# Kernel tuning notes

Hardware: AMD Instinct MI355X
Metric: run time of the kernel (lower is better)

Reference implementation:

```python
import jax, jax.numpy as jnp
import numpy as np

B, S, D, H, SKG = 4, 1024, 1024, 16, 256
HD = D // H  # head dim = 64


def setup_inputs() -> dict:
    key = jax.random.key(0)
    ks = jax.random.split(key, 8)
    std = 0.02
    return {
        "x": jax.random.normal(ks[0], (B, S, D), dtype=jnp.float32),
        "pred_kg": jax.random.normal(ks[1], (B, SKG, D), dtype=jnp.float32),
        "Wc": jax.random.normal(ks[2], (D, 3 * D), dtype=jnp.float32) * std,  # c_attn weight
        "bc": jnp.zeros((3 * D,), dtype=jnp.float32),
        "Wk": jax.random.normal(ks[3], (D, 2 * D), dtype=jnp.float32) * std,  # k_attn weight
        "bk": jnp.zeros((2 * D,), dtype=jnp.float32),
        "Wp": jax.random.normal(ks[4], (D, D), dtype=jnp.float32) * std,     # c_proj weight (shared)
        "bp": jnp.zeros((D,), dtype=jnp.float32),
    }


def _split_heads(t):  # [B, T, D] -> [B, H, T, HD]
    Bb, T, _ = t.shape
    return t.reshape(Bb, T, H, HD).transpose(0, 2, 1, 3)


def _merge_heads(t):  # [B, H, T, HD] -> [B, T, D]
    Bb, _, T, _ = t.shape
    return t.transpose(0, 2, 1, 3).reshape(Bb, T, D)


def reference(x, pred_kg, Wc, bc, Wk, bk, Wp, bp):
    # ---- self-attention branch (GPT-2 style, explicit causal bias blend) ----
    qkv = x @ Wc + bc                       # Conv1D: [B,S,3D]
    q, k, v = jnp.split(qkv, 3, axis=-1)
    q = _split_heads(q)                     # [B,H,S,HD]
    k = _split_heads(k)
    v = _split_heads(v)

    inv_sqrt_d = 1.0 / jnp.sqrt(jnp.float32(HD))
    w = jnp.einsum("bhqd,bhkd->bhqk", q, k) * inv_sqrt_d  # [B,H,S,S]
    causal = jnp.tril(jnp.ones((S, S), dtype=w.dtype))    # bias buffer slice b
    # faithful to: w = w * b - 10000.0 * (1 - b)
    w = w * causal - 10000.0 * (1.0 - causal)
    w = jax.nn.softmax(w, axis=-1)
    a = jnp.einsum("bhqk,bhkd->bhqd", w, v)
    a = _merge_heads(a) @ Wp + bp           # c_proj; resid dropout is identity in eval

    # ---- KG cross-attention branch (shares query and c_proj) ----
    kkv = pred_kg @ Wk + bk                 # [B,SKG,2D]
    kk, kv = jnp.split(kkv, 2, axis=-1)
    kk = _split_heads(kk)                   # [B,H,SKG,HD]
    kv = _split_heads(kv)
    w2 = jnp.einsum("bhqd,bhkd->bhqk", q, kk) * inv_sqrt_d  # [B,H,S,SKG]
    w2 = jax.nn.softmax(w2, axis=-1)
    ka = jnp.einsum("bhqk,bhkd->bhqd", w2, kv)
    ka = _merge_heads(ka) @ Wp + bp

    # concat the two branch outputs along the sequence axis: [B, S+SKG, D]
    return jnp.concatenate([a, ka], axis=1)
```

## Files before the change

kernel.cpp:

```cpp
#include <hip/hip_runtime.h>
#include <hip/hip_bf16.h>

typedef __bf16 bf16_t;
typedef bf16_t bf16x8 __attribute__((ext_vector_type(8)));
typedef bf16_t bf16x4 __attribute__((ext_vector_type(4)));
typedef float f32x4 __attribute__((ext_vector_type(4)));
typedef float f32x16 __attribute__((ext_vector_type(16)));

#define EXP2C 0.1803368867f
#define FEXP2(x) __builtin_amdgcn_exp2f(x)

__device__ __forceinline__ void gload16(const void* g, void* l) {
  __builtin_amdgcn_global_load_lds(
      (const __attribute__((address_space(1))) void*)g,
      (__attribute__((address_space(3))) void*)l, 16, 0, 0);
}

__device__ __forceinline__ unsigned pkbf(float lo, float hi) {
  unsigned short a = __builtin_bit_cast(unsigned short, (bf16_t)lo);
  unsigned short b = __builtin_bit_cast(unsigned short, (bf16_t)hi);
  return (unsigned)a | ((unsigned)b << 16);
}

__device__ __forceinline__ void plswap(unsigned& a, unsigned& b) {
#if __has_builtin(__builtin_amdgcn_permlane32_swap)
  auto r = __builtin_amdgcn_permlane32_swap(a, b, false, false);
  a = r[0]; b = r[1];
#else
  asm("v_permlane32_swap_b32 %0, %1" : "+v"(a), "+v"(b));
#endif
}
__device__ __forceinline__ float xmax32(float x) {
  unsigned a = __builtin_bit_cast(unsigned, x), b = a;
  plswap(a, b);
  return fmaxf(__builtin_bit_cast(float, a), __builtin_bit_cast(float, b));
}
__device__ __forceinline__ float xsum32(float x) {
  unsigned a = __builtin_bit_cast(unsigned, x), b = a;
  plswap(a, b);
  return __builtin_bit_cast(float, a) + __builtin_bit_cast(float, b);
}

__global__ __launch_bounds__(256) void prep_kernel(
    const float* __restrict__ x, bf16_t* __restrict__ xb,
    const float* __restrict__ pkg, bf16_t* __restrict__ pkb,
    const float* __restrict__ Wc, bf16_t* __restrict__ Wct,
    const float* __restrict__ Wk, bf16_t* __restrict__ Wkt,
    const float* __restrict__ Wp, bf16_t* __restrict__ Wpt) {
  __shared__ float tile[32][33];
  const int bid = blockIdx.x, tid = threadIdx.x;
  if (bid < 5120) {
    int i = bid * 256 + tid;
    const float* src; bf16_t* dst;
    if (i < 1048576) { src = x; dst = xb; }
    else { i -= 1048576; src = pkg; dst = pkb; }
    float4 v = reinterpret_cast<const float4*>(src)[i];
    bf16x4 o = { (bf16_t)v.x, (bf16_t)v.y, (bf16_t)v.z, (bf16_t)v.w };
    reinterpret_cast<bf16x4*>(dst)[i] = o;
    return;
  }
  int r = bid - 5120;
  int xx = r % 192, ky = r / 192;
  const float* W; bf16_t* T; int N;
  if (xx < 96) { W = Wc; T = Wct; N = 3072; }
  else if (xx < 160) { W = Wk; T = Wkt; N = 2048; xx -= 96; }
  else { W = Wp; T = Wpt; N = 1024; xx -= 160; }
  const int K = 1024;
  int tx = tid & 31, ty = tid >> 5;
  int n0 = xx * 32, k0 = ky * 32;
#pragma unroll
  for (int i = 0; i < 4; ++i)
    tile[ty + i * 8][tx] = W[(size_t)(k0 + ty + i * 8) * N + n0 + tx];
  __syncthreads();
#pragma unroll
  for (int i = 0; i < 4; ++i)
    T[(size_t)(n0 + ty + i * 8) * K + k0 + tx] = (bf16_t)tile[tx][ty + i * 8];
}

__global__ __launch_bounds__(256) void pack2_kernel(
    const bf16_t* __restrict__ src0, bf16_t* __restrict__ kd0, bf16_t* __restrict__ vd0,
    const bf16_t* __restrict__ src1, bf16_t* __restrict__ kd1, bf16_t* __restrict__ vd1) {
  __shared__ bf16_t vt[32][72];
  const int tid = threadIdx.x;
  int x = blockIdx.x;
  const int bh = blockIdx.y;
  const bf16_t* src; bf16_t *kd, *vd; int R, stride, kcol, vcol, NT, t;
  if (x < 32) { src = src0; kd = kd0; vd = vd0; R = 1024; stride = 3072; kcol = 1024; vcol = 2048; NT = 32; t = x; }
  else        { src = src1; kd = kd1; vd = vd1; R = 256;  stride = 2048; kcol = 0;    vcol = 1024; NT = 8;  t = x - 32; }
  const int b = bh >> 4, h = bh & 15;
  const size_t srow = (size_t)b * R + t * 32;
  const size_t obase = ((size_t)bh * NT + t) * 2048;
  {
    int r = tid >> 3, c = tid & 7;
    bf16x8 d = *(const bf16x8*)&src[(srow + r) * stride + vcol + h * 64 + c * 8];
    *(bf16x8*)&vt[r][c * 8] = d;
  }
  {
    int ks = tid >> 6, l = tid & 63;
    int hi8 = (l >> 5) * 8;
    bf16x8 d = *(const bf16x8*)&src[(srow + (l & 31)) * stride + kcol + h * 64 + ks * 16 + hi8];
    *(bf16x8*)&kd[obase + ks * 512 + l * 8] = d;
  }
  __syncthreads();
  {
    int dd = tid >> 6, l = tid & 63;
    int mb = dd >> 1, ks = dd & 1;
    int hd = mb * 32 + (l & 31);
    int kvr = ks * 16 + (l >> 5) * 8;
    bf16x8 o;
#pragma unroll
    for (int j = 0; j < 8; ++j) o[j] = vt[kvr + j][hd];
    *(bf16x8*)&vd[obase + dd * 512 + l * 8] = o;
  }
}

#define MFMA2(mi, ni)                                                         \
  acc[mi][ni] = __builtin_amdgcn_mfma_f32_16x16x32_bf16(af[(mi) & 1][0], bf[ni][0], acc[mi][ni], 0, 0, 0); \
  acc[mi][ni] = __builtin_amdgcn_mfma_f32_16x16x32_bf16(af[(mi) & 1][1], bf[ni][1], acc[mi][ni], 0, 0, 0);
#define MFMA8(qm, qn)                                                         \
  MFMA2(2 * (qm) + 0, 2 * (qn) + 0) MFMA2(2 * (qm) + 0, 2 * (qn) + 1)         \
  MFMA2(2 * (qm) + 1, 2 * (qn) + 0) MFMA2(2 * (qm) + 1, 2 * (qn) + 1)
#define GBAR() __builtin_amdgcn_s_barrier()
#define LGKM0() asm volatile("s_waitcnt lgkmcnt(0)" ::: "memory")

template <int OUTF32>
__device__ __forceinline__ void gemm8_body(
    char* smem, const bf16_t* __restrict__ A, const bf16_t* __restrict__ Bt,
    const float* __restrict__ bias, void* __restrict__ Cout,
    int N, int K, int bx, int by) {
  const int tid = threadIdx.x;
  const int l = tid & 63, w = tid >> 6;
  const int lr = l & 15, lg = l >> 4;
  const int m0 = by * 256, n0 = bx * 128;
  const int wr = (w >> 1) * 64, wc = (w & 1) * 64;

  const int sr = tid >> 3;
  const int scb = ((tid & 7) * 16) ^ ((sr & 7) << 4);
  const bf16_t* Ab = A + (size_t)m0 * K + (scb >> 1);
  const bf16_t* Bb = Bt + (size_t)n0 * K + (scb >> 1);
  const int nk = K >> 6;

  const int hA = w >> 2;
  const int rA = ((w >> 1) & 1) * 64 + lr;
  const int rB = wc + lr;
  const int xr = (lr & 7) << 4;

  auto STAGE_A = [&](int t, int h) {
    const bf16_t* g = Ab + (size_t)(h * 128 + sr) * K + t * 64;
    char* d = smem + ((size_t)(t & 1) * 2 + h) * 16384 + tid * 16;
    gload16(g, d);
    gload16(g + (size_t)64 * K, d + 8192);
  };
  auto STAGE_B = [&](int t) {
    const bf16_t* g = Bb + (size_t)sr * K + t * 64;
    char* d = smem + 65536 + (size_t)(t & 1) * 16384 + tid * 16;
    gload16(g, d);
    gload16(g + (size_t)64 * K, d + 8192);
  };

  f32x4 acc[4][4] = {};
  bf16x8 af[2][2], bf[4][2];

  STAGE_A(0, 0); STAGE_A(0, 1); STAGE_B(0); STAGE_B(1); STAGE_A(1, 0);
  asm volatile("s_waitcnt vmcnt(4)" ::: "memory");
  GBAR();

  for (int t = 0; t < nk; ++t) {
    const char* pA = smem + ((size_t)(t & 1) * 2 + hA) * 16384;
    const char* pB = smem + 65536 + (size_t)(t & 1) * 16384;
    auto LDA = [&](int mf, int ks) {
      return *(const bf16x8*)(pA + (rA + mf * 16) * 128 + ((ks * 64 + lg * 16) ^ xr));
    };
    auto LDB = [&](int nf, int ks) {
      return *(const bf16x8*)(pB + (rB + nf * 16) * 128 + ((ks * 64 + lg * 16) ^ xr));
    };
    af[0][0] = LDA(0, 0); af[0][1] = LDA(0, 1);
    af[1][0] = LDA(1, 0); af[1][1] = LDA(1, 1);
    bf[0][0] = LDB(0, 0); bf[0][1] = LDB(0, 1);
    bf[1][0] = LDB(1, 0); bf[1][1] = LDB(1, 1);
    if (t + 1 < nk) STAGE_A(t + 1, 1);
    GBAR(); LGKM0();
    __builtin_amdgcn_s_setprio(1);
    MFMA8(0, 0)
    __builtin_amdgcn_s_setprio(0);
    GBAR();
    bf[2][0] = LDB(2, 0); bf[2][1] = LDB(2, 1);
    bf[3][0] = LDB(3, 0); bf[3][1] = LDB(3, 1);
    GBAR(); LGKM0();
    __builtin_amdgcn_s_setprio(1);
    MFMA8(0, 1)
    __builtin_amdgcn_s_setprio(0);
    GBAR();
    af[0][0] = LDA(2, 0); af[0][1] = LDA(2, 1);
    af[1][0] = LDA(3, 0); af[1][1] = LDA(3, 1);
    if (t + 2 < nk) STAGE_B(t + 2);
    GBAR(); LGKM0();
    __builtin_amdgcn_s_setprio(1);
    MFMA8(1, 0)
    __builtin_amdgcn_s_setprio(0);
    GBAR();
    if (t + 2 < nk) STAGE_A(t + 2, 0);
    GBAR();
    __builtin_amdgcn_s_setprio(1);
    MFMA8(1, 1)
    __builtin_amdgcn_s_setprio(0);
    if (t + 2 < nk)      asm volatile("s_waitcnt vmcnt(4)" ::: "memory");
    else if (t + 1 < nk) asm volatile("s_waitcnt vmcnt(0)" ::: "memory");
    GBAR();
  }

#pragma unroll
  for (int mf = 0; mf < 4; ++mf) {
#pragma unroll
    for (int nf = 0; nf < 4; ++nf) {
      int col = n0 + wc + nf * 16 + lr;
      float bb = bias[col];
      int rowb = m0 + wr + mf * 16 + lg * 4;
#pragma unroll
      for (int r = 0; r < 4; ++r) {
        float v = acc[mf][nf][r] + bb;
        if constexpr (OUTF32)
          ((float*)Cout)[(size_t)(rowb + r) * N + col] = v;
        else
          ((bf16_t*)Cout)[(size_t)(rowb + r) * N + col] = (bf16_t)v;
      }
    }
  }
}

__global__ __launch_bounds__(512, 1) void gemm2_kernel(
    const bf16_t* __restrict__ A0, const bf16_t* __restrict__ B0,
    const float* __restrict__ bi0, bf16_t* __restrict__ C0,
    const bf16_t* __restrict__ A1, const bf16_t* __restrict__ B1,
    const float* __restrict__ bi1, bf16_t* __restrict__ C1) {
  extern __shared__ char smem[];
  int bid = blockIdx.x;
  int wg = (bid & 7) * 56 + (bid >> 3);
  if (wg < 384)
    gemm8_body<0>(smem, A0, B0, bi0, C0, 3072, 1024, wg % 24, wg / 24);
  else {
    int r = wg - 384;
    gemm8_body<0>(smem, A1, B1, bi1, C1, 2048, 1024, r % 16, r / 16);
  }
}

__global__ __launch_bounds__(512, 1) void gemm_proj_kernel(
    const bf16_t* __restrict__ A, const bf16_t* __restrict__ Bt,
    const float* __restrict__ bias, float* __restrict__ Cout) {
  extern __shared__ char smem[];
  int bid = blockIdx.x;
  int wg = (bid & 7) * 32 + (bid >> 3);
  gemm8_body<1>(smem, A, Bt, bias, Cout, 1024, 1024, wg % 8, wg / 8);
}

#define STAGE(bf, t)                                                         \
  {                                                                          \
    gload16(kba + (size_t)(t) * 2048 + tid * 8, &sKV[bf][tid * 16]);         \
    gload16(vba + (size_t)(t) * 2048 + tid * 8, &sKV[bf][4096 + tid * 16]);  \
  }
#define QKT()                                                                \
  {                                                                          \
    __builtin_amdgcn_s_setprio(1);                                           \
    _Pragma("unroll") for (int ks = 0; ks < 4; ++ks)                         \
        sa = __builtin_amdgcn_mfma_f32_32x32x16_bf16(kf[ks], qf[ks], sa, 0, 0, 0); \
    __builtin_amdgcn_s_setprio(0);                                           \
  }
#define SMPV(vf, tcur)                                                       \
  {                                                                          \
    float sv[16];                                                            \
    const bool mt = is_self && ((tcur) == qw);                               \
    _Pragma("unroll") for (int r = 0; r < 16; ++r) {                         \
      float v = sa[r];                                                       \
      if (mt) {                                                              \
        int kvr = (r & 3) + 8 * (r >> 2) + kv4;                              \
        v = (kvr > ql) ? -1e30f : v;                                         \
      }                                                                      \
      sv[r] = v;                                                             \
    }                                                                        \
    float tm = fmaxf(                                                        \
        fmaxf(fmaxf(fmaxf(sv[0], sv[1]), fmaxf(sv[2], sv[3])),               \
              fmaxf(fmaxf(sv[4], sv[5]), fmaxf(sv[6], sv[7]))),              \
        fmaxf(fmaxf(fmaxf(sv[8], sv[9]), fmaxf(sv[10], sv[11])),             \
              fmaxf(fmaxf(sv[12], sv[13]), fmaxf(sv[14], sv[15]))));         \
    tm = xmax32(tm);                                                         \
    if (!__all(tm <= mcur + 64.f)) {                                         \
      float mn = fmaxf(mcur, tm);                                            \
      float sc = FEXP2((mcur - mn) * EXP2C);                                 \
      mcur = mn;                                                             \
      lcur *= sc;                                                            \
      _Pragma("unroll") for (int mb = 0; mb < 2; ++mb)                       \
          _Pragma("unroll") for (int r = 0; r < 16; ++r) oacc[mb][r] *= sc;  \
    }                                                                        \
    const float hm = mcur * EXP2C;                                           \
    float pf[16];                                                            \
    _Pragma("unroll") for (int r = 0; r < 16; ++r)                           \
        pf[r] = FEXP2(__builtin_fmaf(sv[r], EXP2C, -hm));                    \
    float ps = (((pf[0] + pf[1]) + (pf[2] + pf[3])) +                        \
                ((pf[4] + pf[5]) + (pf[6] + pf[7]))) +                       \
               (((pf[8] + pf[9]) + (pf[10] + pf[11])) +                      \
                ((pf[12] + pf[13]) + (pf[14] + pf[15])));                    \
    ps = xsum32(ps);                                                         \
    lcur += ps;                                                              \
    unsigned o01 = pkbf(pf[0], pf[1]), o23 = pkbf(pf[2], pf[3]);             \
    unsigned o45 = pkbf(pf[4], pf[5]), o67 = pkbf(pf[6], pf[7]);             \
    unsigned o89 = pkbf(pf[8], pf[9]), o1011 = pkbf(pf[10], pf[11]);         \
    unsigned o1213 = pkbf(pf[12], pf[13]), o1415 = pkbf(pf[14], pf[15]);     \
    plswap(o01, o45); plswap(o23, o67);                                      \
    plswap(o89, o1213); plswap(o1011, o1415);                                \
    uint4 w0 = { o01, o23, o45, o67 };                                       \
    uint4 w1 = { o89, o1011, o1213, o1415 };                                 \
    bf16x8 pb0 = __builtin_bit_cast(bf16x8, w0);                             \
    bf16x8 pb1 = __builtin_bit_cast(bf16x8, w1);                             \
    __builtin_amdgcn_s_setprio(1);                                           \
    oacc[0] = __builtin_amdgcn_mfma_f32_32x32x16_bf16(vf[0], pb0, oacc[0], 0, 0, 0); \
    oacc[0] = __builtin_amdgcn_mfma_f32_32x32x16_bf16(vf[1], pb1, oacc[0], 0, 0, 0); \
    oacc[1] = __builtin_amdgcn_mfma_f32_32x32x16_bf16(vf[2], pb0, oacc[1], 0, 0, 0); \
    oacc[1] = __builtin_amdgcn_mfma_f32_32x32x16_bf16(vf[3], pb1, oacc[1], 0, 0, 0); \
    __builtin_amdgcn_s_setprio(0);                                           \
  }

__global__ __launch_bounds__(256) void attn_kernel(
    const bf16_t* __restrict__ qkv,
    const bf16_t* __restrict__ kfs, const bf16_t* __restrict__ vfs,
    const bf16_t* __restrict__ kfc, const bf16_t* __restrict__ vfc,
    bf16_t* __restrict__ obuf) {
  __shared__ __align__(16) char sKV[3][8192];

  const int tid = threadIdx.x;
  const int w = tid >> 6, l = tid & 63;
  const int ql = l & 31;
  const bool uhi = l >= 32;
  const int kv4 = uhi ? 4 : 0;
  const int hi8 = uhi ? 8 : 0;

  const int bid = blockIdx.x;
  const bool is_self = bid < 512;
  int qb, bh, nt;
  if (is_self) {
    qb = 7 - (bid >> 6);
    bh = bid & 63;
    nt = qb * 4 + 4;
  } else {
    int cb = bid - 512;
    qb = cb >> 6;
    bh = cb & 63;
    nt = 8;
  }
  const int qw = qb * 4 + w;
  const int b = bh >> 4, h = bh & 15;
  const int hcol = h * 64;
  const int q0 = qw * 32;
  const int tlim = is_self ? qw : (nt - 1);

  const bf16_t* kba; const bf16_t* vba; int ooff;
  if (is_self) {
    kba = kfs + (size_t)bh * 32 * 2048; vba = vfs + (size_t)bh * 32 * 2048; ooff = 0;
  } else {
    kba = kfc + (size_t)bh * 8 * 2048;  vba = vfc + (size_t)bh * 8 * 2048;  ooff = 1024;
  }

  const bf16_t* qrow = qkv + (size_t)(b * 1024 + q0 + ql) * 3072 + hcol + hi8;
  bf16x8 qf[4];
#pragma unroll
  for (int ks = 0; ks < 4; ++ks) qf[ks] = *(const bf16x8*)(qrow + ks * 16);

  float mcur = -1e30f, lcur = 0.f;
  f32x16 oacc[2] = {};

  STAGE(0, 0); STAGE(1, 1);
  asm volatile("s_waitcnt vmcnt(2)" ::: "memory");
  __builtin_amdgcn_s_barrier();

  int cur = 0;
  for (int t = 0; t < nt; ++t) {
    int s2 = cur + 2; if (s2 >= 3) s2 -= 3;
    if (t + 2 < nt) STAGE(s2, t + 2);
    if (t <= tlim) {
      bf16x8 kf[4], vf[4];
#pragma unroll
      for (int c = 0; c < 4; ++c)
        kf[c] = *(const bf16x8*)&sKV[cur][c * 1024 + l * 16];
#pragma unroll
      for (int c = 0; c < 4; ++c)
        vf[c] = *(const bf16x8*)&sKV[cur][4096 + c * 1024 + l * 16];
      f32x16 sa = {};
      QKT();
      SMPV(vf, t);
    }
    if (t + 2 < nt)      asm volatile("s_waitcnt vmcnt(2)" ::: "memory");
    else if (t + 1 < nt) asm volatile("s_waitcnt vmcnt(0)" ::: "memory");
    __builtin_amdgcn_s_barrier();
    cur = cur + 1; if (cur >= 3) cur -= 3;
  }
  __syncthreads();

  const float rl = 1.0f / lcur;
  char* swp = &sKV[0][0] + w * 4096;
#pragma unroll
  for (int mb = 0; mb < 2; ++mb)
#pragma unroll
    for (int r2 = 0; r2 < 8; ++r2) {
      float lo = oacc[mb][2 * r2] * rl;
      float hiv = oacc[mb][2 * r2 + 1] * rl;
      int hdb = (r2 & 1) * 2 + 8 * (r2 >> 1) + kv4 + mb * 32;
      int off = (ql * 128 + hdb * 2) ^ ((ql & 7) << 4);
      *(unsigned*)(swp + off) = pkbf(lo, hiv);
    }
  __syncthreads();
  const int orow = b * 2048 + ooff + q0;
#pragma unroll
  for (int it = 0; it < 4; ++it) {
    int idx = it * 64 + l;
    int q = idx >> 3, ch = idx & 7;
    int off = (q * 128 + ch * 16) ^ ((q & 7) << 4);
    uint4 d = *(uint4*)(swp + off);
    *(uint4*)&obuf[(size_t)(orow + q) * 1024 + hcol + ch * 8] = d;
  }
}

extern "C" void kernel_launch(void* const* d_in, const int* in_sizes, int n_in,
                              void* d_out, int out_size, void* d_ws, size_t ws_size,
                              hipStream_t stream) {
  (void)in_sizes; (void)n_in; (void)out_size; (void)ws_size;
  const float* x   = (const float*)d_in[0];
  const float* pkg = (const float*)d_in[1];
  const float* Wc  = (const float*)d_in[2];
  const float* bc  = (const float*)d_in[3];
  const float* Wk  = (const float*)d_in[4];
  const float* bk  = (const float*)d_in[5];
  const float* Wp  = (const float*)d_in[6];
  const float* bp  = (const float*)d_in[7];
  float* out = (float*)d_out;

  char* ws = (char*)d_ws;
  const size_t MB = 1u << 20;
  bf16_t* xb   = (bf16_t*)(ws + 0 * MB);
  bf16_t* pkb  = (bf16_t*)(ws + 8 * MB);
  bf16_t* Wct  = (bf16_t*)(ws + 10 * MB);
  bf16_t* Wkt  = (bf16_t*)(ws + 16 * MB);
  bf16_t* Wpt  = (bf16_t*)(ws + 20 * MB);
  bf16_t* kkvb = (bf16_t*)(ws + 22 * MB);
  bf16_t* abuf = (bf16_t*)(ws + 26 * MB);
  bf16_t* vfs  = (bf16_t*)(ws + 0 * MB);
  bf16_t* kfc  = (bf16_t*)(ws + 8 * MB);
  bf16_t* vfc  = (bf16_t*)(ws + 10 * MB);
  bf16_t* qkvb = (bf16_t*)d_out;
  bf16_t* kfs  = (bf16_t*)((char*)d_out + 24 * MB);

  prep_kernel<<<11264, 256, 0, stream>>>(x, xb, pkg, pkb, Wc, Wct, Wk, Wkt, Wp, Wpt);
  gemm2_kernel<<<448, 512, 98304, stream>>>(xb, Wct, bc, qkvb, pkb, Wkt, bk, kkvb);
  pack2_kernel<<<dim3(40, 64), 256, 0, stream>>>(qkvb, kfs, vfs, kkvb, kfc, vfc);
  attn_kernel<<<1024, 256, 0, stream>>>(qkvb, kfs, vfs, kfc, vfc, abuf);
  gemm_proj_kernel<<<256, 512, 98304, stream>>>(abuf, Wpt, bp, out);
}
```

Measured before the change: 114.7 us.

## Use 256x256 tiles for the QKV and KG projection GEMM

Replaces the 256x128-tile GEMM used for the fused QKV/KKV projection with a new 256x256-tile body. Each wave computes a 128x64 sub-tile in four quadrant phases, staging A and B halves into double-buffered LDS with prioritized MFMA sections. The grid halves from 448 to 224 workgroups and LDS grows to 128KB. The larger tile raises arithmetic intensity and cuts redundant global loads, but 224 blocks is fewer than the 256 CUs on MI355X, so some CUs sit idle.

After: 110.6 us. -3.6%, faster.

```diff
diff --git a/kernel.cpp b/kernel.cpp
--- a/kernel.cpp
+++ b/kernel.cpp
@@ -114,14 +114,150 @@
   }
 }
 
+#define GBAR() __builtin_amdgcn_s_barrier()
+#define LGKM0() asm volatile("s_waitcnt lgkmcnt(0)" ::: "memory")
+
+__device__ __forceinline__ void gemm256_body(
+    char* smem, const bf16_t* __restrict__ A, const bf16_t* __restrict__ Bt,
+    const float* __restrict__ bias, bf16_t* __restrict__ Cout,
+    int N, int K, int bx, int by) {
+  const int tid = threadIdx.x;
+  const int l = tid & 63, w = tid >> 6;
+  const int lr = l & 15, lg = l >> 4;
+  const int m0 = by * 256, n0 = bx * 256;
+  const int wr = (w >> 2) * 128, wc = (w & 3) * 64;
+  const int hA = w >> 2, hB = (w >> 1) & 1;
+
+  const int sr = tid >> 3;
+  const int scb = ((tid & 7) * 16) ^ ((sr & 7) << 4);
+  const bf16_t* Ab = A + (size_t)m0 * K + (scb >> 1);
+  const bf16_t* Bb = Bt + (size_t)n0 * K + (scb >> 1);
+  const int nk = K >> 6;
+  const int xr = (lr & 7) << 4;
+
+  auto STAGE_A = [&](int t, int h) {
+    const bf16_t* g = Ab + (size_t)(h * 128 + sr) * K + t * 64;
+    char* d = smem + ((size_t)(t & 1) * 2 + h) * 16384 + tid * 16;
+    gload16(g, d);
+    gload16(g + (size_t)64 * K, d + 8192);
+  };
+  auto STAGE_B = [&](int t, int h) {
+    const bf16_t* g = Bb + (size_t)(h * 128 + sr) * K + t * 64;
+    char* d = smem + 65536 + ((size_t)(t & 1) * 2 + h) * 16384 + tid * 16;
+    gload16(g, d);
+    gload16(g + (size_t)64 * K, d + 8192);
+  };
+
+  f32x4 acc[8][4] = {};
+  bf16x8 af[4][2], bf[2][2][2];
+
+  STAGE_A(0, 0); STAGE_A(0, 1); STAGE_B(0, 0); STAGE_B(0, 1);
+  asm volatile("s_waitcnt vmcnt(0)" ::: "memory");
+  GBAR();
+
+  for (int t = 0; t < nk; ++t) {
+    const char* pA = smem + ((size_t)(t & 1) * 2 + hA) * 16384;
+    const char* pB = smem + 65536 + ((size_t)(t & 1) * 2 + hB) * 16384;
+    auto LDA = [&](int mf, int ks) {
+      return *(const bf16x8*)(pA + (mf * 16 + lr) * 128 + ((ks * 64 + lg * 16) ^ xr));
+    };
+    auto LDB = [&](int nf, int ks) {
+      return *(const bf16x8*)(pB + ((w & 1) * 64 + nf * 16 + lr) * 128 + ((ks * 64 + lg * 16) ^ xr));
+    };
+#pragma unroll
+    for (int mf = 0; mf < 4; ++mf) { af[mf][0] = LDA(mf, 0); af[mf][1] = LDA(mf, 1); }
+#pragma unroll
+    for (int nf = 0; nf < 2; ++nf) { bf[0][nf][0] = LDB(nf, 0); bf[0][nf][1] = LDB(nf, 1); }
+    if (t + 1 < nk) { STAGE_A(t + 1, 0); STAGE_B(t + 1, 0); }
+    GBAR(); LGKM0();
+    __builtin_amdgcn_s_setprio(1);
+#pragma unroll
+    for (int mf = 0; mf < 4; ++mf)
+#pragma unroll
+      for (int nf = 0; nf < 2; ++nf) {
+        acc[mf][nf] = __builtin_amdgcn_mfma_f32_16x16x32_bf16(af[mf][0], bf[0][nf][0], acc[mf][nf], 0, 0, 0);
+        acc[mf][nf] = __builtin_amdgcn_mfma_f32_16x16x32_bf16(af[mf][1], bf[0][nf][1], acc[mf][nf], 0, 0, 0);
+      }
+    __builtin_amdgcn_s_setprio(0);
+    GBAR();
+#pragma unroll
+    for (int nf = 0; nf < 2; ++nf) { bf[1][nf][0] = LDB(2 + nf, 0); bf[1][nf][1] = LDB(2 + nf, 1); }
+    if (t + 1 < nk) { STAGE_A(t + 1, 1); STAGE_B(t + 1, 1); }
+    GBAR(); LGKM0();
+    __builtin_amdgcn_s_setprio(1);
+#pragma unroll
+    for (int mf = 0; mf < 4; ++mf)
+#pragma unroll
+      for (int nf = 0; nf < 2; ++nf) {
+        acc[mf][2 + nf] = __builtin_amdgcn_mfma_f32_16x16x32_bf16(af[mf][0], bf[1][nf][0], acc[mf][2 + nf], 0, 0, 0);
+        acc[mf][2 + nf] = __builtin_amdgcn_mfma_f32_16x16x32_bf16(af[mf][1], bf[1][nf][1], acc[mf][2 + nf], 0, 0, 0);
+      }
+    __builtin_amdgcn_s_setprio(0);
+    GBAR();
+#pragma unroll
+    for (int mf = 0; mf < 4; ++mf) { af[mf][0] = LDA(4 + mf, 0); af[mf][1] = LDA(4 + mf, 1); }
+    GBAR(); LGKM0();
+    __builtin_amdgcn_s_setprio(1);
+#pragma unroll
+    for (int mf = 0; mf < 4; ++mf)
+#pragma unroll
+      for (int nf = 0; nf < 2; ++nf) {
+        acc[4 + mf][nf] = __builtin_amdgcn_mfma_f32_16x16x32_bf16(af[mf][0], bf[0][nf][0], acc[4 + mf][nf], 0, 0, 0);
+        acc[4 + mf][nf] = __builtin_amdgcn_mfma_f32_16x16x32_bf16(af[mf][1], bf[0][nf][1], acc[4 + mf][nf], 0, 0, 0);
+      }
+    __builtin_amdgcn_s_setprio(0);
+    GBAR();
+    __builtin_amdgcn_s_setprio(1);
+#pragma unroll
+    for (int mf = 0; mf < 4; ++mf)
+#pragma unroll
+      for (int nf = 0; nf < 2; ++nf) {
+        acc[4 + mf][2 + nf] = __builtin_amdgcn_mfma_f32_16x16x32_bf16(af[mf][0], bf[1][nf][0], acc[4 + mf][2 + nf], 0, 0, 0);
+        acc[4 + mf][2 + nf] = __builtin_amdgcn_mfma_f32_16x16x32_bf16(af[mf][1], bf[1][nf][1], acc[4 + mf][2 + nf], 0, 0, 0);
+      }
+    __builtin_amdgcn_s_setprio(0);
+    asm volatile("s_waitcnt vmcnt(0)" ::: "memory");
+    GBAR();
+  }
+
+#pragma unroll
+  for (int mf = 0; mf < 8; ++mf) {
+#pragma unroll
+    for (int nf = 0; nf < 4; ++nf) {
+      int col = n0 + wc + nf * 16 + lr;
+      float bb = bias[col];
+      int rowb = m0 + wr + mf * 16 + lg * 4;
+#pragma unroll
+      for (int r = 0; r < 4; ++r) {
+        float v = acc[mf][nf][r] + bb;
+        ((bf16_t*)Cout)[(size_t)(rowb + r) * N + col] = (bf16_t)v;
+      }
+    }
+  }
+}
+
+__global__ __launch_bounds__(512, 1) void gemm2_kernel(
+    const bf16_t* __restrict__ A0, const bf16_t* __restrict__ B0,
+    const float* __restrict__ bi0, bf16_t* __restrict__ C0,
+    const bf16_t* __restrict__ A1, const bf16_t* __restrict__ B1,
+    const float* __restrict__ bi1, bf16_t* __restrict__ C1) {
+  extern __shared__ char smem[];
+  int bid = blockIdx.x;
+  int wg = (bid & 7) * 28 + (bid >> 3);
+  if (wg < 192)
+    gemm256_body(smem, A0, B0, bi0, C0, 3072, 1024, wg % 12, wg / 12);
+  else {
+    int r = wg - 192;
+    gemm256_body(smem, A1, B1, bi1, C1, 2048, 1024, r % 8, r / 8);
+  }
+}
+
 #define MFMA2(mi, ni)                                                         \
   acc[mi][ni] = __builtin_amdgcn_mfma_f32_16x16x32_bf16(af[(mi) & 1][0], bf[ni][0], acc[mi][ni], 0, 0, 0); \
   acc[mi][ni] = __builtin_amdgcn_mfma_f32_16x16x32_bf16(af[(mi) & 1][1], bf[ni][1], acc[mi][ni], 0, 0, 0);
 #define MFMA8(qm, qn)                                                         \
   MFMA2(2 * (qm) + 0, 2 * (qn) + 0) MFMA2(2 * (qm) + 0, 2 * (qn) + 1)         \
   MFMA2(2 * (qm) + 1, 2 * (qn) + 0) MFMA2(2 * (qm) + 1, 2 * (qn) + 1)
-#define GBAR() __builtin_amdgcn_s_barrier()
-#define LGKM0() asm volatile("s_waitcnt lgkmcnt(0)" ::: "memory")
 
 template <int OUTF32>
 __device__ __forceinline__ void gemm8_body(
@@ -225,22 +361,6 @@
           ((bf16_t*)Cout)[(size_t)(rowb + r) * N + col] = (bf16_t)v;
       }
     }
-  }
-}
-
-__global__ __launch_bounds__(512, 1) void gemm2_kernel(
-    const bf16_t* __restrict__ A0, const bf16_t* __restrict__ B0,
-    const float* __restrict__ bi0, bf16_t* __restrict__ C0,
-    const bf16_t* __restrict__ A1, const bf16_t* __restrict__ B1,
-    const float* __restrict__ bi1, bf16_t* __restrict__ C1) {
-  extern __shared__ char smem[];
-  int bid = blockIdx.x;
-  int wg = (bid & 7) * 56 + (bid >> 3);
-  if (wg < 384)
-    gemm8_body<0>(smem, A0, B0, bi0, C0, 3072, 1024, wg % 24, wg / 24);
-  else {
-    int r = wg - 384;
-    gemm8_body<0>(smem, A1, B1, bi1, C1, 2048, 1024, r % 16, r / 16);
   }
 }
 
@@ -448,7 +568,7 @@
   bf16_t* kfs  = (bf16_t*)((char*)d_out + 24 * MB);
 
   prep_kernel<<<11264, 256, 0, stream>>>(x, xb, pkg, pkb, Wc, Wct, Wk, Wkt, Wp, Wpt);
-  gemm2_kernel<<<448, 512, 98304, stream>>>(xb, Wct, bc, qkvb, pkb, Wkt, bk, kkvb);
+  gemm2_kernel<<<224, 512, 131072, stream>>>(xb, Wct, bc, qkvb, pkb, Wkt, bk, kkvb);
   pack2_kernel<<<dim3(40, 64), 256, 0, stream>>>(qkvb, kfs, vfs, kkvb, kfc, vfc);
   attn_kernel<<<1024, 256, 0, stream>>>(qkvb, kfs, vfs, kfc, vfc, abuf);
   gemm_proj_kernel<<<256, 512, 98304, stream>>>(abuf, Wpt, bp, out);
```
